# Kernel tuning notes

Measured on AMD Instinct MI355X. Metric: run time of the kernel, lower is better.

## Reference

```python
import jax, jax.numpy as jnp
import numpy as np

B, T, C = 64, 2048, 32
OUT_T = 2048

def setup_inputs() -> dict:
    key = jax.random.key(0)
    k1, k2 = jax.random.split(key)
    X = jax.random.normal(k1, (B, T, C), dtype=jnp.float32)
    # small init so deformations are modest displacements, like a trained locnet
    W_loc = jax.random.normal(k2, (T * C, OUT_T), dtype=jnp.float32) * 1e-3
    b_loc = jnp.zeros((OUT_T,), dtype=jnp.float32)
    return {"X": X, "W_loc": W_loc, "b_loc": b_loc}

def reference(X, W_loc, b_loc):
    b, t, c = X.shape
    out_t = W_loc.shape[1]
    # localization net: flatten + dense -> per-output-point displacement (B, OUT_T)
    deformation = X.reshape(b, t * c) @ W_loc + b_loc
    # sampling grid: linspace(0, T-1, OUT_T), shared across batch, shifted by deformation
    grid = jnp.linspace(0.0, jnp.float32(t - 1), out_t)  # (OUT_T,)
    x = grid[None, :] + deformation                       # (B, OUT_T) float sample coords
    # linear interpolation with clamped integer neighbors
    x0 = jnp.floor(x).astype(jnp.int32)
    x1 = x0 + 1
    x0c = jnp.clip(x0, 0, t - 1)
    x1c = jnp.clip(x1, 0, t - 1)
    batch_idx = jnp.arange(b)[:, None]                    # (B, 1)
    v0 = X[batch_idx, x0c]                                # (B, OUT_T, C) gather along T
    v1 = X[batch_idx, x1c]                                # (B, OUT_T, C)
    # weights use the CLIPPED coords cast back to float (faithful to original)
    w0 = (x1c.astype(x.dtype) - x)[..., None]             # (B, OUT_T, 1)
    w1 = (x - x0c.astype(x.dtype))[..., None]
    return w0 * v0 + w1 * v1                              # (B, OUT_T, C)
```

## Files before the change

kernel.cpp:

```cpp
#include <hip/hip_runtime.h>
#include <hip/hip_bf16.h>
#include <stdint.h>

constexpr int BATCH = 64;
constexpr int T     = 2048;
constexpr int CCH   = 32;
constexpr int OUT_T = 2048;
constexpr int K     = T * CCH;
constexpr int N     = OUT_T;

constexpr int TN     = 64;
constexpr int NBN    = N / TN;
constexpr int KSPLIT = 64;
constexpr int CK     = K / KSPLIT;
constexpr int BK     = 32;
constexpr int NS     = CK / BK;

typedef __attribute__((ext_vector_type(8))) short short8;
typedef __attribute__((ext_vector_type(4))) float f32x4;

__device__ __forceinline__ void split_bf16(float x, ushort& h, ushort& l) {
  unsigned xb = __float_as_uint(x);
  h = (ushort)(xb >> 16);
  float hf = __uint_as_float(xb & 0xFFFF0000u);
  float lf = x - hf;
  unsigned u = __float_as_uint(lf);
  unsigned r = u + 0x7FFFu + ((u >> 16) & 1u);
  l = (ushort)(r >> 16);
}

__global__ __launch_bounds__(256) void gemm_split_kernel(
    const float* __restrict__ X,
    const float* __restrict__ W,
    float* __restrict__ def) {
  const int bid = blockIdx.x;
  const int lb  = (bid & 7) * 256 + (bid >> 3);
  const int bn  = lb & (NBN - 1);
  const int bk  = lb >> 5;

  const int tid  = threadIdx.x;
  const int lane = tid & 63;
  const int wave = tid >> 6;
  const int r = lane & 15;
  const int g = lane >> 4;

  __shared__ ushort Ahi[2][64][32];
  __shared__ ushort Alo[2][64][32];
  __shared__ ushort Bhi[2][64][40];
  __shared__ ushort Blo[2][64][40];

  f32x4 acc[4] = {};

  const int kbase = bk * CK;

  float4 aReg[2];
  float  bReg[2][4];

  auto issue_loads = [&](int ks) {
    const int k0 = kbase + ks * BK;
#pragma unroll
    for (int it = 0; it < 2; ++it) {
      int flat = it * 256 + tid;
      int m  = flat >> 3;
      int kq = flat & 7;
      aReg[it] = *(const float4*)&X[(size_t)m * K + k0 + kq * 4];
    }
#pragma unroll
    for (int it = 0; it < 2; ++it) {
      int flat = it * 256 + tid;
      int n  = flat & 63;
      int kq = flat >> 6;
      const float* wp = &W[(size_t)(k0 + kq * 4) * N + bn * TN + n];
      bReg[it][0] = wp[0];
      bReg[it][1] = wp[N];
      bReg[it][2] = wp[2 * N];
      bReg[it][3] = wp[3 * N];
    }
  };

  auto stage = [&](int buf) {
#pragma unroll
    for (int it = 0; it < 2; ++it) {
      int flat = it * 256 + tid;
      int m  = flat >> 3;
      int kq = flat & 7;
      const float4 v = aReg[it];
      ushort h0, h1, h2, h3, l0, l1, l2, l3;
      split_bf16(v.x, h0, l0); split_bf16(v.y, h1, l1);
      split_bf16(v.z, h2, l2); split_bf16(v.w, h3, l3);
      uint2 ph; ph.x = (unsigned)h0 | ((unsigned)h1 << 16);
                ph.y = (unsigned)h2 | ((unsigned)h3 << 16);
      uint2 pl; pl.x = (unsigned)l0 | ((unsigned)l1 << 16);
                pl.y = (unsigned)l2 | ((unsigned)l3 << 16);
      *(uint2*)&Ahi[buf][m][kq * 4] = ph;
      *(uint2*)&Alo[buf][m][kq * 4] = pl;
    }
#pragma unroll
    for (int it = 0; it < 2; ++it) {
      int flat = it * 256 + tid;
      int n  = flat & 63;
      int kq = flat >> 6;
      ushort h0, h1, h2, h3, l0, l1, l2, l3;
      split_bf16(bReg[it][0], h0, l0); split_bf16(bReg[it][1], h1, l1);
      split_bf16(bReg[it][2], h2, l2); split_bf16(bReg[it][3], h3, l3);
      uint2 ph; ph.x = (unsigned)h0 | ((unsigned)h1 << 16);
                ph.y = (unsigned)h2 | ((unsigned)h3 << 16);
      uint2 pl; pl.x = (unsigned)l0 | ((unsigned)l1 << 16);
                pl.y = (unsigned)l2 | ((unsigned)l3 << 16);
      *(uint2*)&Bhi[buf][n][kq * 4] = ph;
      *(uint2*)&Blo[buf][n][kq * 4] = pl;
    }
  };

  issue_loads(0);
  stage(0);
  __syncthreads();

  for (int ks = 0; ks < NS; ++ks) {
    const int cur = ks & 1;
    if (ks + 1 < NS) issue_loads(ks + 1);

    short8 bh = *(const short8*)&Bhi[cur][wave * 16 + r][g * 8];
    short8 bl = *(const short8*)&Blo[cur][wave * 16 + r][g * 8];
#pragma unroll
    for (int mf = 0; mf < 4; ++mf) {
      short8 ah = *(const short8*)&Ahi[cur][mf * 16 + r][g * 8];
      short8 al = *(const short8*)&Alo[cur][mf * 16 + r][g * 8];
      acc[mf] = __builtin_amdgcn_mfma_f32_16x16x32_bf16(ah, bh, acc[mf], 0, 0, 0);
      acc[mf] = __builtin_amdgcn_mfma_f32_16x16x32_bf16(ah, bl, acc[mf], 0, 0, 0);
      acc[mf] = __builtin_amdgcn_mfma_f32_16x16x32_bf16(al, bh, acc[mf], 0, 0, 0);
    }

    if (ks + 1 < NS) stage(cur ^ 1);
    __syncthreads();
  }

  const int ncol = bn * TN + wave * 16 + r;
#pragma unroll
  for (int mf = 0; mf < 4; ++mf) {
    const int mbase = mf * 16 + g * 4;
#pragma unroll
    for (int q = 0; q < 4; ++q) {
      atomicAdd(&def[(size_t)(mbase + q) * N + ncol], acc[mf][q]);
    }
  }
}

__global__ __launch_bounds__(256) void resample_kernel(
    const float* __restrict__ X,
    const float* __restrict__ def,
    const float* __restrict__ b_loc,
    float* __restrict__ out) {
  const int tid = blockIdx.x * 256 + threadIdx.x;
  const int c4 = tid & 7;
  const int o  = (tid >> 3) & (OUT_T - 1);
  const int b  = tid >> 14;

  const float x = (float)o + def[b * OUT_T + o] + b_loc[o];
  const float xf = floorf(x);
  const int x0 = (int)xf;
  const int x1 = x0 + 1;
  const int x0c = min(max(x0, 0), T - 1);
  const int x1c = min(max(x1, 0), T - 1);
  const float w0 = (float)x1c - x;
  const float w1 = x - (float)x0c;

  const float4 v0 = *(const float4*)&X[((size_t)b * T + x0c) * CCH + c4 * 4];
  const float4 v1 = *(const float4*)&X[((size_t)b * T + x1c) * CCH + c4 * 4];
  float4 res;
  res.x = w0 * v0.x + w1 * v1.x;
  res.y = w0 * v0.y + w1 * v1.y;
  res.z = w0 * v0.z + w1 * v1.z;
  res.w = w0 * v0.w + w1 * v1.w;
  *(float4*)&out[((size_t)b * OUT_T + o) * CCH + c4 * 4] = res;
}

extern "C" void kernel_launch(void* const* d_in, const int* in_sizes, int n_in,
                              void* d_out, int out_size, void* d_ws, size_t ws_size,
                              hipStream_t stream) {
  const float* X     = (const float*)d_in[0];
  const float* W     = (const float*)d_in[1];
  const float* b_loc = (const float*)d_in[2];
  float* out = (float*)d_out;
  float* def = (float*)d_ws;

  hipMemsetAsync(def, 0, (size_t)BATCH * N * sizeof(float), stream);

  dim3 gblk(NBN * KSPLIT);
  gemm_split_kernel<<<gblk, 256, 0, stream>>>(X, W, def);

  dim3 rblk((BATCH * OUT_T * 8) / 256);
  resample_kernel<<<rblk, 256, 0, stream>>>(X, def, b_loc, out);
}
```

Baseline: 709.2 us.

## Pre-split X into bf16 hi/lo buffers and stream A fragments directly from global

Adds a pre-pass kernel that splits X into bf16 high and low halves once, so the GEMM no longer redoes the split for every N tile. The GEMM now loads A fragments straight from global memory into registers, skipping LDS for A, and uses a two-stage register prefetch for W with an unrolled ping-pong loop. It also halves KSPLIT, which means fewer atomics and workgroups but longer per-block K loops, and it uses a bf16 conversion intrinsic for the low half. In exchange it adds an extra kernel plus workspace traffic for Xhi and Xlo, and the uncoalesced per-lane global A loads could cost bandwidth.

```diff
diff --git a/kernel.cpp b/kernel.cpp
--- a/kernel.cpp
+++ b/kernel.cpp
@@ -11,30 +11,44 @@
 
 constexpr int TN     = 64;
 constexpr int NBN    = N / TN;
-constexpr int KSPLIT = 64;
+constexpr int KSPLIT = 32;
 constexpr int CK     = K / KSPLIT;
 constexpr int BK     = 32;
 constexpr int NS     = CK / BK;
+constexpr int NWG    = NBN * KSPLIT;
 
 typedef __attribute__((ext_vector_type(8))) short short8;
 typedef __attribute__((ext_vector_type(4))) float f32x4;
 
-__device__ __forceinline__ void split_bf16(float x, ushort& h, ushort& l) {
-  unsigned xb = __float_as_uint(x);
-  h = (ushort)(xb >> 16);
-  float hf = __uint_as_float(xb & 0xFFFF0000u);
-  float lf = x - hf;
-  unsigned u = __float_as_uint(lf);
-  unsigned r = u + 0x7FFFu + ((u >> 16) & 1u);
-  l = (ushort)(r >> 16);
+__device__ __forceinline__ void split2t(float a, float b, unsigned& hpk, unsigned& lpk) {
+  unsigned ua = __float_as_uint(a), ub = __float_as_uint(b);
+  hpk = (ua >> 16) | (ub & 0xFFFF0000u);
+  float la = a - __uint_as_float(ua & 0xFFFF0000u);
+  float lb = b - __uint_as_float(ub & 0xFFFF0000u);
+  __hip_bfloat162 l2 = __float22bfloat162_rn(make_float2(la, lb));
+  __builtin_memcpy(&lpk, &l2, 4);
+}
+
+__global__ __launch_bounds__(256) void xsplit_kernel(
+    const float* __restrict__ X, ushort* __restrict__ Xhi, ushort* __restrict__ Xlo) {
+  const int i = blockIdx.x * 256 + threadIdx.x;
+  const float4 v = ((const float4*)X)[i];
+  unsigned h01, l01, h23, l23;
+  split2t(v.x, v.y, h01, l01);
+  split2t(v.z, v.w, h23, l23);
+  uint2 hv; hv.x = h01; hv.y = h23;
+  uint2 lv; lv.x = l01; lv.y = l23;
+  ((uint2*)Xhi)[i] = hv;
+  ((uint2*)Xlo)[i] = lv;
 }
 
 __global__ __launch_bounds__(256) void gemm_split_kernel(
-    const float* __restrict__ X,
-    const float* __restrict__ W,
+    const ushort* __restrict__ Xhi,
+    const ushort* __restrict__ Xlo,
+    const float*  __restrict__ W,
     float* __restrict__ def) {
   const int bid = blockIdx.x;
-  const int lb  = (bid & 7) * 256 + (bid >> 3);
+  const int lb  = (bid & 7) * (NWG / 8) + (bid >> 3);
   const int bn  = lb & (NBN - 1);
   const int bk  = lb >> 5;
 
@@ -44,94 +58,87 @@
   const int r = lane & 15;
   const int g = lane >> 4;
 
-  __shared__ ushort Ahi[2][64][32];
-  __shared__ ushort Alo[2][64][32];
   __shared__ ushort Bhi[2][64][40];
   __shared__ ushort Blo[2][64][40];
 
   f32x4 acc[4] = {};
-
   const int kbase = bk * CK;
 
-  float4 aReg[2];
-  float  bReg[2][4];
-
-  auto issue_loads = [&](int ks) {
+  unsigned aOff[4];
+#pragma unroll
+  for (int mf = 0; mf < 4; ++mf)
+    aOff[mf] = (unsigned)((mf * 16 + r) * (K * 2) + (kbase + 8 * g) * 2);
+
+  auto issueA = [&](short8 (&ah)[4], short8 (&al)[4]) {
+#pragma unroll
+    for (int mf = 0; mf < 4; ++mf) {
+      ah[mf] = *(const short8*)((const char*)Xhi + aOff[mf]);
+      al[mf] = *(const short8*)((const char*)Xlo + aOff[mf]);
+    }
+#pragma unroll
+    for (int mf = 0; mf < 4; ++mf) aOff[mf] += BK * 2;
+  };
+
+  auto issueB = [&](int ks, float (&bb)[8]) {
     const int k0 = kbase + ks * BK;
-#pragma unroll
-    for (int it = 0; it < 2; ++it) {
-      int flat = it * 256 + tid;
-      int m  = flat >> 3;
-      int kq = flat & 7;
-      aReg[it] = *(const float4*)&X[(size_t)m * K + k0 + kq * 4];
-    }
 #pragma unroll
     for (int it = 0; it < 2; ++it) {
       int flat = it * 256 + tid;
       int n  = flat & 63;
       int kq = flat >> 6;
       const float* wp = &W[(size_t)(k0 + kq * 4) * N + bn * TN + n];
-      bReg[it][0] = wp[0];
-      bReg[it][1] = wp[N];
-      bReg[it][2] = wp[2 * N];
-      bReg[it][3] = wp[3 * N];
-    }
-  };
-
-  auto stage = [&](int buf) {
-#pragma unroll
-    for (int it = 0; it < 2; ++it) {
-      int flat = it * 256 + tid;
-      int m  = flat >> 3;
-      int kq = flat & 7;
-      const float4 v = aReg[it];
-      ushort h0, h1, h2, h3, l0, l1, l2, l3;
-      split_bf16(v.x, h0, l0); split_bf16(v.y, h1, l1);
-      split_bf16(v.z, h2, l2); split_bf16(v.w, h3, l3);
-      uint2 ph; ph.x = (unsigned)h0 | ((unsigned)h1 << 16);
-                ph.y = (unsigned)h2 | ((unsigned)h3 << 16);
-      uint2 pl; pl.x = (unsigned)l0 | ((unsigned)l1 << 16);
-                pl.y = (unsigned)l2 | ((unsigned)l3 << 16);
-      *(uint2*)&Ahi[buf][m][kq * 4] = ph;
-      *(uint2*)&Alo[buf][m][kq * 4] = pl;
-    }
+#pragma unroll
+      for (int j = 0; j < 4; ++j) bb[it * 4 + j] = wp[(size_t)j * N];
+    }
+  };
+
+  auto stageB = [&](int buf, float (&bb)[8]) {
 #pragma unroll
     for (int it = 0; it < 2; ++it) {
       int flat = it * 256 + tid;
       int n  = flat & 63;
       int kq = flat >> 6;
-      ushort h0, h1, h2, h3, l0, l1, l2, l3;
-      split_bf16(bReg[it][0], h0, l0); split_bf16(bReg[it][1], h1, l1);
-      split_bf16(bReg[it][2], h2, l2); split_bf16(bReg[it][3], h3, l3);
-      uint2 ph; ph.x = (unsigned)h0 | ((unsigned)h1 << 16);
-                ph.y = (unsigned)h2 | ((unsigned)h3 << 16);
-      uint2 pl; pl.x = (unsigned)l0 | ((unsigned)l1 << 16);
-                pl.y = (unsigned)l2 | ((unsigned)l3 << 16);
-      *(uint2*)&Bhi[buf][n][kq * 4] = ph;
-      *(uint2*)&Blo[buf][n][kq * 4] = pl;
-    }
-  };
-
-  issue_loads(0);
-  stage(0);
+      unsigned h01, l01, h23, l23;
+      split2t(bb[it * 4 + 0], bb[it * 4 + 1], h01, l01);
+      split2t(bb[it * 4 + 2], bb[it * 4 + 3], h23, l23);
+      uint2 hv; hv.x = h01; hv.y = h23;
+      uint2 lv; lv.x = l01; lv.y = l23;
+      *(uint2*)&Bhi[buf][n][kq * 4] = hv;
+      *(uint2*)&Blo[buf][n][kq * 4] = lv;
+    }
+  };
+
+  auto mfma_step = [&](int buf, short8 (&ah)[4], short8 (&al)[4]) {
+    short8 bh = *(const short8*)&Bhi[buf][wave * 16 + r][g * 8];
+    short8 bl = *(const short8*)&Blo[buf][wave * 16 + r][g * 8];
+#pragma unroll
+    for (int mf = 0; mf < 4; ++mf) {
+      acc[mf] = __builtin_amdgcn_mfma_f32_16x16x32_bf16(ah[mf], bh, acc[mf], 0, 0, 0);
+      acc[mf] = __builtin_amdgcn_mfma_f32_16x16x32_bf16(ah[mf], bl, acc[mf], 0, 0, 0);
+      acc[mf] = __builtin_amdgcn_mfma_f32_16x16x32_bf16(al[mf], bh, acc[mf], 0, 0, 0);
+    }
+  };
+
+  short8 aCh[4], aCl[4], aNh[4], aNl[4];
+  float bReg0[8], bReg1[8];
+
+  issueB(0, bReg0);
+  issueB(1, bReg1);
+  issueA(aCh, aCl);
+  stageB(0, bReg0);
   __syncthreads();
 
-  for (int ks = 0; ks < NS; ++ks) {
-    const int cur = ks & 1;
-    if (ks + 1 < NS) issue_loads(ks + 1);
-
-    short8 bh = *(const short8*)&Bhi[cur][wave * 16 + r][g * 8];
-    short8 bl = *(const short8*)&Blo[cur][wave * 16 + r][g * 8];
-#pragma unroll
-    for (int mf = 0; mf < 4; ++mf) {
-      short8 ah = *(const short8*)&Ahi[cur][mf * 16 + r][g * 8];
-      short8 al = *(const short8*)&Alo[cur][mf * 16 + r][g * 8];
-      acc[mf] = __builtin_amdgcn_mfma_f32_16x16x32_bf16(ah, bh, acc[mf], 0, 0, 0);
-      acc[mf] = __builtin_amdgcn_mfma_f32_16x16x32_bf16(ah, bl, acc[mf], 0, 0, 0);
-      acc[mf] = __builtin_amdgcn_mfma_f32_16x16x32_bf16(al, bh, acc[mf], 0, 0, 0);
-    }
-
-    if (ks + 1 < NS) stage(cur ^ 1);
+  for (int t = 0; t < NS; t += 2) {
+    issueA(aNh, aNl);
+    if (t + 2 < NS) issueB(t + 2, bReg0);
+    mfma_step(0, aCh, aCl);
+    stageB(1, bReg1);
+    __syncthreads();
+
+    if (t + 2 < NS) issueA(aCh, aCl);
+    if (t + 3 < NS) issueB(t + 3, bReg1);
+    mfma_step(1, aNh, aNl);
+    if (t + 2 < NS) stageB(0, bReg0);
     __syncthreads();
   }
 
@@ -182,13 +189,16 @@
   const float* W     = (const float*)d_in[1];
   const float* b_loc = (const float*)d_in[2];
   float* out = (float*)d_out;
-  float* def = (float*)d_ws;
+
+  float*  def = (float*)d_ws;
+  ushort* Xhi = (ushort*)((char*)d_ws + (1u << 20));
+  ushort* Xlo = (ushort*)((char*)d_ws + (1u << 20) + (size_t)BATCH * K * 2);
 
   hipMemsetAsync(def, 0, (size_t)BATCH * N * sizeof(float), stream);
 
-  dim3 gblk(NBN * KSPLIT);
-  gemm_split_kernel<<<gblk, 256, 0, stream>>>(X, W, def);
-
-  dim3 rblk((BATCH * OUT_T * 8) / 256);
-  resample_kernel<<<rblk, 256, 0, stream>>>(X, def, b_loc, out);
-}
+  xsplit_kernel<<<(BATCH * K / 4) / 256, 256, 0, stream>>>(X, Xhi, Xlo);
+
+  gemm_split_kernel<<<NWG, 256, 0, stream>>>(Xhi, Xlo, W, def);
+
+  resample_kernel<<<(BATCH * OUT_T * 8) / 256, 256, 0, stream>>>(X, def, b_loc, out);
+}
```

Measured after the change: 863.4 us. 1.22x slower.
